# Kernel tuning notes

Hardware: AMD Instinct MI355X
Metric: run time of the kernel (lower is better)

## Reference

```python
import jax, jax.numpy as jnp
import numpy as np

NH = 8      # num_head
WIN = 7     # window
EPS = 1e-6


def _ln(x, w, b):
    m = x.mean(-1, keepdims=True)
    v = ((x - m) ** 2).mean(-1, keepdims=True)
    return (x - m) / jnp.sqrt(v + EPS) * w + b


def _dwconv(x, w, b):
    # x: [B,H,W,Cc], w: [7,7,1,Cc] (HWIO), depthwise (groups=Cc)
    y = jax.lax.conv_general_dilated(
        x, w, window_strides=(1, 1), padding='SAME',
        dimension_numbers=('NHWC', 'HWIO', 'NHWC'),
        feature_group_count=x.shape[-1])
    return y + b


def setup_inputs() -> dict:
    B, H, W, C = 16, 56, 56, 256
    RATIO = 8
    key = jax.random.key(0)
    ki = iter(jax.random.split(key, 48))
    def lin(i, o):
        return jax.random.normal(next(ki), (i, o), jnp.float32) * (1.0 / i) ** 0.5
    def bias(o):
        return jnp.zeros((o,), jnp.float32)
    def dw(c):
        return jax.random.normal(next(ki), (7, 7, 1, c), jnp.float32) * 0.05
    inp = {
        'x':   jax.random.normal(next(ki), (B, H, W, C), jnp.float32),
        'x_e': jax.random.normal(next(ki), (B, H, W, C // 2), jnp.float32),
        # LayerNorms
        'norm_w': jnp.ones((C,), jnp.float32),  'norm_b': bias(C),
        'norme_w': jnp.ones((C // 2,), jnp.float32), 'norme_b': bias(C // 2),
        # local_rr path
        'rr1_w': lin(C, C), 'rr1_b': bias(C),
        'rr2_w': lin(C, C), 'rr2_b': bias(C),
        'rr3_w': lin(C, C), 'rr3_b': bias(C),
        'conv_w': dw(C), 'conv_b': bias(C),
        # LocalAttentionRGBT
        'lx_l1_w': lin(C, C // 2), 'lx_l1_b': bias(C // 2),
        'lx_l2_w': lin(C // 2, C // 2), 'lx_l2_b': bias(C // 2),
        'lx_c1_w': dw(C // 2), 'lx_c1_b': bias(C // 2),
        'lx_c2_w': dw(C // 2), 'lx_c2_b': bias(C // 2),
        'lx_fc1_w': lin(C, C // RATIO),  # no bias
        'lx_fc2_w': lin(C // RATIO, C),  # no bias
        'lx_l3_w': lin(C, C // 2), 'lx_l3_b': bias(C // 2),
        # global pooled attention
        'kv_w': lin(C, C), 'kv_b': bias(C),
        'q_w': lin(C // 2 * 3, C // 2), 'q_b': bias(C // 2),
        # output projections (window != 0 => in = 2C)
        'proj_w': lin(2 * C, C), 'proj_b': bias(C),
        'proje_w': lin(2 * C, C // 2), 'proje_b': bias(C // 2),
    }
    return inp


def reference(x, x_e, norm_w, norm_b, norme_w, norme_b,
              rr1_w, rr1_b, rr2_w, rr2_b, rr3_w, rr3_b, conv_w, conv_b,
              lx_l1_w, lx_l1_b, lx_l2_w, lx_l2_b, lx_c1_w, lx_c1_b,
              lx_c2_w, lx_c2_b, lx_fc1_w, lx_fc2_w, lx_l3_w, lx_l3_b,
              kv_w, kv_b, q_w, q_b, proj_w, proj_b, proje_w, proje_b):
    B, H, W, C = x.shape
    hd = C // NH // 2  # head dim
    x = _ln(x, norm_w, norm_b)
    x_e = _ln(x_e, norme_w, norme_b)

    # --- local_rr: gated depthwise-conv branch ---
    rr1 = x @ rr1_w + rr1_b
    rr2 = _dwconv(x @ rr2_w + rr2_b, conv_w, conv_b)
    rr2 = rr2 @ rr3_w + rr3_b
    local_rr = rr1 * rr2  # [B,H,W,C]

    # --- LocalAttentionRGBT: cross-modal cosine-sim channel gate ---
    rgb = x @ lx_l1_w + lx_l1_b      # [B,H,W,C/2]
    t = x_e @ lx_l2_w + lx_l2_b      # [B,H,W,C/2]
    co = _dwconv(rgb * t, lx_c1_w, lx_c1_b)
    di = _dwconv(jnp.abs(rgb - t), lx_c2_w, lx_c2_b)
    co_di = jnp.concatenate([co, di], axis=-1)           # [B,H,W,C]
    amap = co_di.mean(-1, keepdims=True)                 # [B,H,W,1]
    dot = (amap * co_di).sum((1, 2), keepdims=True)      # [B,1,1,C]
    n1 = jnp.sqrt((amap ** 2).sum((1, 2), keepdims=True))
    n2 = jnp.sqrt((co_di ** 2).sum((1, 2), keepdims=True))
    cos_sim = dot / (n1 * n2 + 1e-6)                     # [B,1,1,C]
    attn_c = jax.nn.sigmoid(
        jax.nn.gelu(cos_sim @ lx_fc1_w, approximate=False) @ lx_fc2_w)
    local_rx = (co_di * attn_c) @ lx_l3_w + lx_l3_b      # [B,H,W,C/2]

    # --- global: pooled-q full-kv attention ---
    kv = (x @ kv_w + kv_b).reshape(B, H * W, 2, NH, hd).transpose(2, 0, 3, 1, 4)
    k, v = kv[0], kv[1]                                  # [B,NH,HW,hd]
    rx = jnp.concatenate([x, x_e], axis=-1)              # [B,H,W,3C/2]
    rx_pool = rx.reshape(B, WIN, H // WIN, WIN, W // WIN, -1).mean((2, 4))  # [B,7,7,3C/2]
    q = (rx_pool @ q_w + q_b).reshape(B, WIN * WIN, NH, hd).transpose(0, 2, 1, 3)
    scores = jnp.einsum('bnqd,bnkd->bnqk', q * hd ** -0.5, k)  # [B,NH,49,HW]
    attn = jax.nn.softmax(scores, axis=-1)
    g = jnp.einsum('bnqk,bnkd->bnqd', attn, v)           # [B,NH,49,hd]
    g = g.reshape(B, NH, WIN, WIN, hd).transpose(0, 1, 4, 2, 3).reshape(B, C // 2, WIN, WIN)
    g = jax.image.resize(g, (B, C // 2, H, W), method='bilinear')  # align_corners=False
    g = g.transpose(0, 2, 3, 1)                          # [B,H,W,C/2]

    cat = jnp.concatenate([local_rr, local_rx, g], axis=-1)  # [B,H,W,2C]
    x_e_out = cat @ proje_w + proje_b
    x_out = cat @ proj_w + proj_b
    return (x_out, x_e_out)
```

## Files before the change

### kernel.cpp

```cpp
#include <hip/hip_runtime.h>
#include <hip/hip_bf16.h>
#include <cstdint>
#include <cstddef>

#define N_TOK 50176
#define HWSZ  3136
#define BATCH 16

#define GF_MUL     1
#define GF_ASCALE  2
#define GF_KVSPLIT 4
#define GF_DUAL    8

typedef __hip_bfloat16 bf16;
typedef __attribute__((ext_vector_type(8))) short bf16x8;
typedef __attribute__((ext_vector_type(4))) float f32x4;
typedef __attribute__((ext_vector_type(4))) unsigned short u16x4;

__device__ __forceinline__ void  stf(float* p, size_t i, float v) { p[i] = v; }
__device__ __forceinline__ void  stf(bf16* p, size_t i, float v) { p[i] = __float2bfloat16(v); }
__device__ __forceinline__ float bu2f(unsigned short u) {
    unsigned int x = ((unsigned int)u) << 16; float f; __builtin_memcpy(&f, &x, 4); return f;
}
__device__ __forceinline__ unsigned short f2bu(float f) {
    bf16 t = __float2bfloat16(f); unsigned short u; __builtin_memcpy(&u, &t, 2); return u;
}

struct WtrDesc { const float* src; bf16* dst; int K; int N; int off; };
struct WtrPack { WtrDesc d[9]; int total; };
__global__ __launch_bounds__(256) void wtr_all(WtrPack p)
{
    int idx = blockIdx.x * 256 + threadIdx.x;
    if (idx >= p.total) return;
    #pragma unroll
    for (int s = 0; s < 9; s++) {
        int lo = p.d[s].off, hi = lo + p.d[s].K * p.d[s].N;
        if (idx >= lo && idx < hi) {
            int j = idx - lo;
            int k = j / p.d[s].N, n = j % p.d[s].N;
            p.d[s].dst[(size_t)n * p.d[s].K + k] = __float2bfloat16(p.d[s].src[j]);
        }
    }
}

__global__ __launch_bounds__(256) void ln_kernel(const float* __restrict__ in,
    const float* __restrict__ w, const float* __restrict__ b,
    bf16* __restrict__ out, int rows, int Cdim)
{
    int wave = threadIdx.x >> 6, lane = threadIdx.x & 63;
    int row = blockIdx.x * 4 + wave;
    if (row >= rows) return;
    const float* p = in + (size_t)row * Cdim;
    int nj = Cdim >> 6;
    float v[4];
    float s = 0.f;
    for (int j = 0; j < nj; j++) { v[j] = p[lane + 64 * j]; s += v[j]; }
    for (int off = 32; off; off >>= 1) s += __shfl_xor(s, off, 64);
    float mean = s / (float)Cdim;
    float vs = 0.f;
    for (int j = 0; j < nj; j++) { float d = v[j] - mean; vs += d * d; }
    for (int off = 32; off; off >>= 1) vs += __shfl_xor(vs, off, 64);
    float rstd = 1.f / sqrtf(vs / (float)Cdim + 1e-6f);
    bf16* q = out + (size_t)row * Cdim;
    for (int j = 0; j < nj; j++) {
        int c = lane + 64 * j;
        q[c] = __float2bfloat16((v[j] - mean) * rstd * w[c] + b[c]);
    }
}

#define LDT 56
template<int FLAGS, typename OT>
__global__ __launch_bounds__(256) void gemm_mfma(
    const bf16* __restrict__ A, int lda,
    const bf16* __restrict__ WT,
    const float* __restrict__ bias,
    OT* __restrict__ C, int ldc,
    int M, int K, int N,
    const bf16* __restrict__ mul, int mulld,
    const float* __restrict__ ascale,
    bf16* __restrict__ kout, bf16* __restrict__ vout,
    OT* __restrict__ C2, int ldc2, const float* __restrict__ bias2, int N1)
{
    __shared__ bf16 As[128][LDT];
    __shared__ bf16 Bs[128][LDT];
    int ntile = N >> 7;
    int m0 = (blockIdx.x / ntile) * 128;
    int n0 = (blockIdx.x % ntile) * 128;
    int tid = threadIdx.x;
    int lane = tid & 63, wid = tid >> 6;
    int wr = (wid >> 1) * 64, wc = (wid & 1) * 64;
    int lrow = lane & 15, lko = (lane >> 4) * 8;
    int sr = tid >> 2, sko = (tid & 3) * 8;

    f32x4 acc[4][4];
    #pragma unroll
    for (int i = 0; i < 4; i++)
        #pragma unroll
        for (int j = 0; j < 4; j++)
            acc[i][j] = (f32x4){0.f, 0.f, 0.f, 0.f};

    bf16x8 ra[2], rb[2];
    #pragma unroll
    for (int i = 0; i < 2; i++) {
        int r = sr + i * 64;
        bf16x8 v = *reinterpret_cast<const bf16x8*>(A + (size_t)(m0 + r) * lda + sko);
        if (FLAGS & GF_ASCALE) {
            int bidx = (m0 + r) / HWSZ;
            const float* as = ascale + (size_t)bidx * K + sko;
            #pragma unroll
            for (int e = 0; e < 8; e++)
                v[e] = (short)f2bu(bu2f((unsigned short)v[e]) * as[e]);
        }
        ra[i] = v;
        rb[i] = *reinterpret_cast<const bf16x8*>(WT + (size_t)(n0 + r) * K + sko);
    }

    for (int k0 = 0; k0 < K; k0 += 32) {
        #pragma unroll
        for (int i = 0; i < 2; i++) {
            *reinterpret_cast<bf16x8*>(&As[sr + i * 64][sko]) = ra[i];
            *reinterpret_cast<bf16x8*>(&Bs[sr + i * 64][sko]) = rb[i];
        }
        __syncthreads();
        int kn = k0 + 32;
        if (kn < K) {
            #pragma unroll
            for (int i = 0; i < 2; i++) {
                int r = sr + i * 64;
                bf16x8 v = *reinterpret_cast<const bf16x8*>(A + (size_t)(m0 + r) * lda + kn + sko);
                if (FLAGS & GF_ASCALE) {
                    int bidx = (m0 + r) / HWSZ;
                    const float* as = ascale + (size_t)bidx * K + kn + sko;
                    #pragma unroll
                    for (int e = 0; e < 8; e++)
                        v[e] = (short)f2bu(bu2f((unsigned short)v[e]) * as[e]);
                }
                ra[i] = v;
                rb[i] = *reinterpret_cast<const bf16x8*>(WT + (size_t)(n0 + r) * K + kn + sko);
            }
        }
        bf16x8 af[4], br[4];
        #pragma unroll
        for (int i = 0; i < 4; i++)
            af[i] = *reinterpret_cast<const bf16x8*>(&As[wr + i * 16 + lrow][lko]);
        #pragma unroll
        for (int j = 0; j < 4; j++)
            br[j] = *reinterpret_cast<const bf16x8*>(&Bs[wc + j * 16 + lrow][lko]);
        #pragma unroll
        for (int i = 0; i < 4; i++)
            #pragma unroll
            for (int j = 0; j < 4; j++)
                acc[i][j] = __builtin_amdgcn_mfma_f32_16x16x32_bf16(af[i], br[j], acc[i][j], 0, 0, 0);
        __syncthreads();
    }

    int orow = (lane >> 4) * 4;
    int ocol = lane & 15;
    #pragma unroll
    for (int i = 0; i < 4; i++) {
        #pragma unroll
        for (int j = 0; j < 4; j++) {
            #pragma unroll
            for (int p = 0; p < 4; p++) {
                int gm = m0 + wr + i * 16 + orow + p;
                int gn = n0 + wc + j * 16 + ocol;
                if (FLAGS & GF_KVSPLIT) {
                    float v = acc[i][j][p] + bias[gn];
                    int bb = gm / HWSZ, n = gm % HWSZ;
                    if (gn < 128)
                        kout[(((size_t)bb * 8 + (gn >> 4)) * HWSZ + n) * 16 + (gn & 15)] = __float2bfloat16(v);
                    else {
                        int hh = (gn - 128) >> 4, dd = (gn - 128) & 15;
                        vout[(((size_t)bb * 8 + hh) * 16 + dd) * HWSZ + n] = __float2bfloat16(v);
                    }
                } else if (FLAGS & GF_DUAL) {
                    if (gn < N1) {
                        float v = acc[i][j][p] + bias[gn];
                        stf(C, (size_t)gm * ldc + gn, v);
                    } else {
                        float v = acc[i][j][p] + bias2[gn - N1];
                        stf(C2, (size_t)gm * ldc2 + (gn - N1), v);
                    }
                } else {
                    float v = acc[i][j][p] + bias[gn];
                    if (FLAGS & GF_MUL) v *= __bfloat162float(mul[(size_t)gm * mulld + gn]);
                    stf(C, (size_t)gm * ldc + gn, v);
                }
            }
        }
    }
}

__global__ __launch_bounds__(256) void gemm_k(
    const float* __restrict__ A, int lda,
    const float* __restrict__ Wt, const float* __restrict__ bias,
    float* __restrict__ Cc, int ldc, int M, int K, int Nc)
{
    __shared__ float As[16][68];
    __shared__ float Ws[16][64];
    int ntile = Nc >> 6;
    int tile_n = blockIdx.x % ntile;
    int tile_m = blockIdx.x / ntile;
    int m0 = tile_m * 64, n0 = tile_n * 64;
    int tid = threadIdx.x;
    int tx = tid & 15, ty = tid >> 4;
    float acc[4][4] = {};
    for (int k0 = 0; k0 < K; k0 += 16) {
        int ks = tid & 15, ms = tid >> 4;
        #pragma unroll
        for (int i = 0; i < 4; i++) {
            int gm = m0 + ms + i * 16;
            As[ks][ms + i * 16] = (gm < M) ? A[(size_t)gm * lda + k0 + ks] : 0.f;
        }
        #pragma unroll
        for (int j = 0; j < 4; j++) {
            int k = (tid >> 6) * 4 + j;
            Ws[k][tid & 63] = Wt[(size_t)(k0 + k) * Nc + n0 + (tid & 63)];
        }
        __syncthreads();
        #pragma unroll
        for (int k = 0; k < 16; k++) {
            float a[4], w[4];
            #pragma unroll
            for (int i = 0; i < 4; i++) a[i] = As[k][ty * 4 + i];
            #pragma unroll
            for (int j = 0; j < 4; j++) w[j] = Ws[k][tx * 4 + j];
            #pragma unroll
            for (int i = 0; i < 4; i++)
                #pragma unroll
                for (int j = 0; j < 4; j++)
                    acc[i][j] += a[i] * w[j];
        }
        __syncthreads();
    }
    #pragma unroll
    for (int i = 0; i < 4; i++) {
        int gm = m0 + ty * 4 + i;
        if (gm >= M) continue;
        #pragma unroll
        for (int j = 0; j < 4; j++) {
            int gn = n0 + tx * 4 + j;
            Cc[(size_t)gm * ldc + gn] = acc[i][j] + bias[gn];
        }
    }
}

__global__ __launch_bounds__(256) void dwconv_reg(const bf16* __restrict__ in,
    bf16* __restrict__ out,
    const float* __restrict__ w0, const float* __restrict__ b0,
    const float* __restrict__ w1, const float* __restrict__ b1, int split)
{
    int tid = threadIdx.x;
    int chg = tid & 31;
    int bsw = (blockIdx.x & 7) * 196 + (blockIdx.x >> 3);
    int pg  = bsw * 8 + (tid >> 5);
    int xg = pg % 14;
    int y  = (pg / 14) % 56;
    int b  = pg / (14 * 56);
    int c0 = chg * 8;
    int x0 = xg * 4;

    const float* wp; const float* bp; int ws, cw;
    if (c0 < split) { wp = w0; bp = b0; ws = split;       cw = c0; }
    else            { wp = w1; bp = b1; ws = 256 - split; cw = c0 - split; }

    float acc[4][8];
    #pragma unroll
    for (int o = 0; o < 4; o++)
        #pragma unroll
        for (int e = 0; e < 8; e++) acc[o][e] = 0.f;

    const bf16* base = in + (size_t)b * HWSZ * 256 + c0;
    const float* wbase = wp + cw;
    #pragma unroll
    for (int ky = 0; ky < 7; ky++) {
        int gy = y + ky - 3;
        if (gy < 0 || gy >= 56) continue;
        const bf16* rowp = base + (size_t)gy * 56 * 256;
        float cf[10][8];
        #pragma unroll
        for (int j = 0; j < 10; j++) {
            int gx = x0 + j - 3;
            bf16x8 v = {0, 0, 0, 0, 0, 0, 0, 0};
            if ((unsigned)gx < 56u)
                v = *reinterpret_cast<const bf16x8*>(rowp + (size_t)gx * 256);
            #pragma unroll
            for (int e = 0; e < 8; e++) cf[j][e] = bu2f((unsigned short)v[e]);
        }
        const float* wrow = wbase + ky * 7 * ws;
        #pragma unroll
        for (int kx = 0; kx < 7; kx++) {
            float4 wa = *reinterpret_cast<const float4*>(wrow + kx * ws);
            float4 wb = *reinterpret_cast<const float4*>(wrow + kx * ws + 4);
            #pragma unroll
            for (int o = 0; o < 4; o++) {
                acc[o][0] += cf[o + kx][0] * wa.x;
                acc[o][1] += cf[o + kx][1] * wa.y;
                acc[o][2] += cf[o + kx][2] * wa.z;
                acc[o][3] += cf[o + kx][3] * wa.w;
                acc[o][4] += cf[o + kx][4] * wb.x;
                acc[o][5] += cf[o + kx][5] * wb.y;
                acc[o][6] += cf[o + kx][6] * wb.z;
                acc[o][7] += cf[o + kx][7] * wb.w;
            }
        }
    }

    float4 ba = *reinterpret_cast<const float4*>(bp + cw);
    float4 bb = *reinterpret_cast<const float4*>(bp + cw + 4);
    bf16* obase = out + (((size_t)b * HWSZ + (size_t)y * 56 + x0) * 256) + c0;
    #pragma unroll
    for (int o = 0; o < 4; o++) {
        bf16x8 ov;
        ov[0] = (short)f2bu(acc[o][0] + ba.x);
        ov[1] = (short)f2bu(acc[o][1] + ba.y);
        ov[2] = (short)f2bu(acc[o][2] + ba.z);
        ov[3] = (short)f2bu(acc[o][3] + ba.w);
        ov[4] = (short)f2bu(acc[o][4] + bb.x);
        ov[5] = (short)f2bu(acc[o][5] + bb.y);
        ov[6] = (short)f2bu(acc[o][6] + bb.z);
        ov[7] = (short)f2bu(acc[o][7] + bb.w);
        *reinterpret_cast<bf16x8*>(obase + (size_t)o * 256) = ov;
    }
}

__global__ void rgbt_k(const bf16* __restrict__ rgb, const bf16* __restrict__ t,
                       bf16* __restrict__ codin, int total )
{
    int i = blockIdx.x * blockDim.x + threadIdx.x;
    if (i >= total) return;
    int n = i >> 7, c = i & 127;
    float a = __bfloat162float(rgb[i]), bb = __bfloat162float(t[i]);
    codin[(size_t)n * 256 + c] = __float2bfloat16(a * bb);
    codin[(size_t)n * 256 + 128 + c] = __float2bfloat16(fabsf(a - bb));
}

__global__ __launch_bounds__(256) void cosred_k(const bf16* __restrict__ codi,
    float* __restrict__ part)
{
    int b = blockIdx.x >> 4;
    int bi = blockIdx.x & 15;
    int wave = threadIdx.x >> 6, lane = threadIdx.x & 63;
    int slot = bi * 4 + wave;
    float dloc[4] = {0,0,0,0}, n2loc[4] = {0,0,0,0};
    float n1loc = 0.f;
    for (int i = 0; i < 49; i++) {
        int p = slot * 49 + i;
        const bf16* row = codi + ((size_t)b * HWSZ + p) * 256;
        float v[4]; float sum = 0.f;
        #pragma unroll
        for (int j = 0; j < 4; j++) { v[j] = __bfloat162float(row[lane + 64 * j]); sum += v[j]; }
        for (int off = 32; off; off >>= 1) sum += __shfl_xor(sum, off, 64);
        float amap = sum * (1.f / 256.f);
        #pragma unroll
        for (int j = 0; j < 4; j++) { dloc[j] += amap * v[j]; n2loc[j] += v[j] * v[j]; }
        n1loc += amap * amap;
    }
    float* dst = part + ((size_t)b * 64 + slot) * 513;
    #pragma unroll
    for (int j = 0; j < 4; j++) {
        dst[lane + 64 * j] = dloc[j];
        dst[256 + lane + 64 * j] = n2loc[j];
    }
    if (lane == 0) dst[512] = n1loc;
}

__global__ __launch_bounds__(256) void mlp_kernel(const float* __restrict__ part,
    const float* __restrict__ fc1w, const float* __restrict__ fc2w,
    float* __restrict__ attnc)
{
    int b = blockIdx.x;
    int tid = threadIdx.x;
    __shared__ float cosb[256];
    __shared__ float hbuf[32];
    const float* pb = part + (size_t)b * 64 * 513;
    float dot = 0.f, n2 = 0.f, n1 = 0.f;
    for (int s = 0; s < 64; s++) {
        dot += pb[s * 513 + tid];
        n2  += pb[s * 513 + 256 + tid];
        n1  += pb[s * 513 + 512];
    }
    float cs = dot / (sqrtf(n1) * sqrtf(n2) + 1e-6f);
    cosb[tid] = cs;
    __syncthreads();
    if (tid < 32) {
        float h = 0.f;
        for (int c = 0; c < 256; c++) h += cosb[c] * fc1w[c * 32 + tid];
        h = 0.5f * h * (1.f + erff(h * 0.70710678f));
        hbuf[tid] = h;
    }
    __syncthreads();
    float o = 0.f;
    for (int j = 0; j < 32; j++) o += hbuf[j] * fc2w[j * 256 + tid];
    attnc[b * 256 + tid] = 1.f / (1.f + expf(-o));
}

__global__ __launch_bounds__(384) void pool_kernel(const bf16* __restrict__ xn,
    const bf16* __restrict__ xen, float* __restrict__ rxpool)
{
    int bij = blockIdx.x;
    int b = bij / 49; int ij = bij % 49; int i = ij / 7, j = ij % 7;
    int c = threadIdx.x;
    float s = 0.f;
    for (int dy = 0; dy < 8; dy++)
        for (int dx = 0; dx < 8; dx++) {
            size_t n = ((size_t)b * 56 + (i * 8 + dy)) * 56 + (j * 8 + dx);
            s += (c < 256) ? __bfloat162float(xn[n * 256 + c])
                           : __bfloat162float(xen[n * 128 + (c - 256)]);
        }
    rxpool[(size_t)bij * 384 + c] = s * (1.f / 64.f);
}

#define NSPLIT 14
#define POSB   224
__global__ __launch_bounds__(256) void attn_mfma(const float* __restrict__ qbuf,
    const bf16* __restrict__ kbuf, const bf16* __restrict__ vtbuf,
    float* __restrict__ osplit, float* __restrict__ mlbuf)
{
    int bh = blockIdx.x & 127;
    int split = blockIdx.x >> 7;
    int b = bh >> 3, h = bh & 7;
    int tid = threadIdx.x;
    int qt = tid >> 6;
    int lane = tid & 63;
    int lo = lane & 15, hi = lane >> 4;

    bf16x8 qf = {0, 0, 0, 0, 0, 0, 0, 0};
    int q = qt * 16 + lo;
    if (hi < 2 && q < 49) {
        const float* qp = qbuf + ((size_t)b * 49 + q) * 128 + h * 16 + hi * 8;
        #pragma unroll
        for (int j = 0; j < 8; j++) qf[j] = (short)f2bu(qp[j] * 0.25f);
    }
    const bf16* kbase = kbuf + (size_t)bh * HWSZ * 16;
    const bf16* vbase = vtbuf + ((size_t)bh * 16 + lo) * HWSZ;

    float m_run = -1e30f, l_run = 0.f;
    f32x4 oacc = {0.f, 0.f, 0.f, 0.f};
    int pos1 = 8 * (lo >> 2) + (lo & 3);
    const f32x4 zz = {0.f, 0.f, 0.f, 0.f};

    for (int t = 0; t < POSB / 32; t++) {
        int base = split * POSB + t * 32;
        bf16x8 kf1 = {0, 0, 0, 0, 0, 0, 0, 0}, kf2 = kf1;
        if (hi < 2) {
            kf1 = *reinterpret_cast<const bf16x8*>(kbase + (size_t)(base + pos1) * 16 + hi * 8);
            kf2 = *reinterpret_cast<const bf16x8*>(kbase + (size_t)(base + pos1 + 4) * 16 + hi * 8);
        }
        bf16x8 vf = *reinterpret_cast<const bf16x8*>(vbase + base + hi * 8);
        f32x4 s1 = __builtin_amdgcn_mfma_f32_16x16x32_bf16(kf1, qf, zz, 0, 0, 0);
        f32x4 s2 = __builtin_amdgcn_mfma_f32_16x16x32_bf16(kf2, qf, zz, 0, 0, 0);
        float pmax = fmaxf(fmaxf(fmaxf(s1[0], s1[1]), fmaxf(s1[2], s1[3])),
                           fmaxf(fmaxf(s2[0], s2[1]), fmaxf(s2[2], s2[3])));
        pmax = fmaxf(pmax, __shfl_xor(pmax, 16, 64));
        pmax = fmaxf(pmax, __shfl_xor(pmax, 32, 64));
        float mnew = fmaxf(m_run, pmax);
        float esc = __expf(m_run - mnew);
        l_run *= esc;
        float e0 = __shfl(esc, 4 * hi + 0, 64);
        float e1 = __shfl(esc, 4 * hi + 1, 64);
        float e2 = __shfl(esc, 4 * hi + 2, 64);
        float e3 = __shfl(esc, 4 * hi + 3, 64);
        oacc[0] *= e0; oacc[1] *= e1; oacc[2] *= e2; oacc[3] *= e3;
        float p0 = __expf(s1[0] - mnew), p1 = __expf(s1[1] - mnew);
        float p2 = __expf(s1[2] - mnew), p3 = __expf(s1[3] - mnew);
        float p4 = __expf(s2[0] - mnew), p5 = __expf(s2[1] - mnew);
        float p6 = __expf(s2[2] - mnew), p7 = __expf(s2[3] - mnew);
        float rs = ((p0 + p1) + (p2 + p3)) + ((p4 + p5) + (p6 + p7));
        rs += __shfl_xor(rs, 16, 64);
        rs += __shfl_xor(rs, 32, 64);
        l_run += rs;
        m_run = mnew;
        bf16x8 pf;
        pf[0] = (short)f2bu(p0); pf[1] = (short)f2bu(p1);
        pf[2] = (short)f2bu(p2); pf[3] = (short)f2bu(p3);
        pf[4] = (short)f2bu(p4); pf[5] = (short)f2bu(p5);
        pf[6] = (short)f2bu(p6); pf[7] = (short)f2bu(p7);
        oacc = __builtin_amdgcn_mfma_f32_16x16x32_bf16(pf, vf, oacc, 0, 0, 0);
    }

    float* ob = osplit + ((size_t)bh * NSPLIT + split) * 64 * 16;
    #pragma unroll
    for (int r = 0; r < 4; r++) {
        int qq = qt * 16 + 4 * hi + r;
        ob[(size_t)qq * 16 + lo] = oacc[r];
    }
    if (hi == 0) {
        float* mlb = mlbuf + (((size_t)bh * NSPLIT + split) * 64 + qt * 16 + lo) * 2;
        mlb[0] = m_run; mlb[1] = l_run;
    }
}

__global__ __launch_bounds__(256) void attn_combine(const float* __restrict__ osplit,
    const float* __restrict__ mlbuf, float* __restrict__ gs)
{
    int idx = blockIdx.x * 256 + threadIdx.x;
    if (idx >= 128 * 49 * 16) return;
    int d = idx & 15;
    int pq = idx >> 4;
    int bh = pq / 49, q = pq % 49;
    float m[NSPLIT], l[NSPLIT];
    float M = -1e30f;
    #pragma unroll
    for (int s = 0; s < NSPLIT; s++) {
        const float* mlb = mlbuf + (((size_t)bh * NSPLIT + s) * 64 + q) * 2;
        m[s] = mlb[0]; l[s] = mlb[1];
        M = fmaxf(M, m[s]);
    }
    float L = 0.f, O = 0.f;
    #pragma unroll
    for (int s = 0; s < NSPLIT; s++) {
        float e = __expf(m[s] - M);
        L += l[s] * e;
        O += osplit[(((size_t)bh * NSPLIT + s) * 64 + q) * 16 + d] * e;
    }
    gs[(size_t)pq * 16 + d] = O / L;
}

__global__ void upsample_kernel(const float* __restrict__ gs, bf16* __restrict__ cat)
{
    int idx = blockIdx.x * blockDim.x + threadIdx.x;
    if (idx >= N_TOK * 128) return;
    int c = idx & 127;
    int pos = idx >> 7;
    int h = c >> 4, d = c & 15;
    int x = pos % 56;
    int y = (pos / 56) % 56;
    int b = pos / HWSZ;
    float sy = (y + 0.5f) * 0.125f - 0.5f;
    float sx = (x + 0.5f) * 0.125f - 0.5f;
    int y0f = (int)floorf(sy); float wy = sy - (float)y0f;
    int x0f = (int)floorf(sx); float wx = sx - (float)x0f;
    int y0 = max(0, min(6, y0f)), y1 = max(0, min(6, y0f + 1));
    int x0 = max(0, min(6, x0f)), x1 = max(0, min(6, x0f + 1));
    const float* g0 = gs + ((size_t)(b * 8 + h) * 49) * 16 + d;
    float v00 = g0[(y0 * 7 + x0) * 16], v01 = g0[(y0 * 7 + x1) * 16];
    float v10 = g0[(y1 * 7 + x0) * 16], v11 = g0[(y1 * 7 + x1) * 16];
    float v0 = v00 + (v01 - v00) * wx;
    float v1 = v10 + (v11 - v10) * wx;
    float v = v0 + (v1 - v0) * wy;
    cat[(size_t)pos * 512 + 384 + c] = __float2bfloat16(v);
}

extern "C" void kernel_launch(void* const* d_in, const int* in_sizes, int n_in,
                              void* d_out, int out_size, void* d_ws, size_t ws_size,
                              hipStream_t stream)
{
    const float* x      = (const float*)d_in[0];
    const float* x_e    = (const float*)d_in[1];
    const float* norm_w = (const float*)d_in[2];
    const float* norm_b = (const float*)d_in[3];
    const float* norme_w= (const float*)d_in[4];
    const float* norme_b= (const float*)d_in[5];
    const float* rr1_w  = (const float*)d_in[6];
    const float* rr1_b  = (const float*)d_in[7];
    const float* rr2_w  = (const float*)d_in[8];
    const float* rr2_b  = (const float*)d_in[9];
    const float* rr3_w  = (const float*)d_in[10];
    const float* rr3_b  = (const float*)d_in[11];
    const float* conv_w = (const float*)d_in[12];
    const float* conv_b = (const float*)d_in[13];
    const float* l1_w   = (const float*)d_in[14];
    const float* l1_b   = (const float*)d_in[15];
    const float* l2_w   = (const float*)d_in[16];
    const float* l2_b   = (const float*)d_in[17];
    const float* c1_w   = (const float*)d_in[18];
    const float* c1_b   = (const float*)d_in[19];
    const float* c2_w   = (const float*)d_in[20];
    const float* c2_b   = (const float*)d_in[21];
    const float* fc1_w  = (const float*)d_in[22];
    const float* fc2_w  = (const float*)d_in[23];
    const float* l3_w   = (const float*)d_in[24];
    const float* l3_b   = (const float*)d_in[25];
    const float* kv_w   = (const float*)d_in[26];
    const float* kv_b   = (const float*)d_in[27];
    const float* q_w    = (const float*)d_in[28];
    const float* q_b    = (const float*)d_in[29];
    const float* proj_w = (const float*)d_in[30];
    const float* proj_b = (const float*)d_in[31];
    const float* proje_w= (const float*)d_in[32];
    const float* proje_b= (const float*)d_in[33];

    float* part   = (float*)d_ws;
    float* attnc  = part   + (size_t)525312;
    float* gs     = attnc  + 4096;
    float* rxpool = gs     + 100352;
    float* qbuf   = rxpool + 301056;
    bf16* wt      = (bf16*)(qbuf + 100352);
    bf16* rr1_t  = wt;
    bf16* rr2_t  = rr1_t + 65536;
    bf16* rr3_t  = rr2_t + 65536;
    bf16* kv_t   = rr3_t + 65536;
    bf16* l1_t   = kv_t  + 65536;
    bf16* l2_t   = l1_t  + 32768;
    bf16* l3_t   = l2_t  + 16384;
    bf16* proj_t = l3_t  + 32768;
    bf16* proje_t= proj_t + 131072;
    bf16* xn     = proje_t + 65536;
    bf16* xen    = xn   + (size_t)N_TOK * 256;
    bf16* bufC   = xen  + (size_t)N_TOK * 128;
    bf16* bufD   = bufC + (size_t)N_TOK * 256;
    bf16* bufE   = bufD + (size_t)N_TOK * 256;
    bf16* cat    = bufE + (size_t)N_TOK * 256;
    size_t need = (size_t)((char*)(cat + (size_t)N_TOK * 512) - (char*)d_ws);
    if (ws_size < need) return;

    bf16* kbuf = bufC;
    bf16* vbuf = bufC + (size_t)N_TOK * 128;

    float* osplit = (float*)bufD;
    float* mlbuf  = osplit + (size_t)128 * NSPLIT * 64 * 16;

    float* xout  = (float*)d_out;
    float* xeout = xout + (size_t)N_TOK * 256;

    const int nthr = 256;
    auto mgrid = [](int M, int N) { return dim3((M / 128) * (N / 128)); };

    {
        WtrPack p;
        const float* srcs[9] = {rr1_w, rr2_w, rr3_w, kv_w, l1_w, l2_w, l3_w, proj_w, proje_w};
        bf16* dsts[9] = {rr1_t, rr2_t, rr3_t, kv_t, l1_t, l2_t, l3_t, proj_t, proje_t};
        int Ks[9] = {256, 256, 256, 256, 256, 128, 256, 512, 512};
        int Ns[9] = {256, 256, 256, 256, 128, 128, 128, 256, 128};
        int off = 0;
        for (int s = 0; s < 9; s++) {
            p.d[s] = {srcs[s], dsts[s], Ks[s], Ns[s], off};
            off += Ks[s] * Ns[s];
        }
        p.total = off;
        wtr_all<<<dim3((off + 255) / 256), dim3(256), 0, stream>>>(p);
    }

    ln_kernel<<<dim3(N_TOK / 4), dim3(nthr), 0, stream>>>(x, norm_w, norm_b, xn, N_TOK, 256);
    ln_kernel<<<dim3(N_TOK / 4), dim3(nthr), 0, stream>>>(x_e, norme_w, norme_b, xen, N_TOK, 128);

    gemm_mfma<GF_DUAL, bf16><<<mgrid(N_TOK, 512), dim3(nthr), 0, stream>>>(
        xn, 256, rr1_t, rr1_b, bufC, 256, N_TOK, 256, 512, nullptr, 0, nullptr, nullptr, nullptr,
        bufD, 256, rr2_b, 256);
    dwconv_reg<<<dim3(N_TOK / 32), dim3(nthr), 0, stream>>>(
        bufD, bufE, conv_w, conv_b, conv_w, conv_b, 256);
    gemm_mfma<GF_MUL, bf16><<<mgrid(N_TOK, 256), dim3(nthr), 0, stream>>>(
        bufE, 256, rr3_t, rr3_b, cat, 512, N_TOK, 256, 256, bufC, 256, nullptr, nullptr, nullptr,
        nullptr, 0, nullptr, 0);

    gemm_mfma<0, bf16><<<mgrid(N_TOK, 128), dim3(nthr), 0, stream>>>(
        xn, 256, l1_t, l1_b, bufD, 128, N_TOK, 256, 128, nullptr, 0, nullptr, nullptr, nullptr,
        nullptr, 0, nullptr, 0);
    gemm_mfma<0, bf16><<<mgrid(N_TOK, 128), dim3(nthr), 0, stream>>>(
        xen, 128, l2_t, l2_b, bufD + (size_t)N_TOK * 128, 128, N_TOK, 128, 128, nullptr, 0, nullptr, nullptr, nullptr,
        nullptr, 0, nullptr, 0);
    rgbt_k<<<dim3((N_TOK * 128) / nthr), dim3(nthr), 0, stream>>>(
        bufD, bufD + (size_t)N_TOK * 128, bufC, N_TOK * 128);
    dwconv_reg<<<dim3(N_TOK / 32), dim3(nthr), 0, stream>>>(
        bufC, bufE, c1_w, c1_b, c2_w, c2_b, 128);
    cosred_k<<<dim3(BATCH * 16), dim3(nthr), 0, stream>>>(bufE, part);
    mlp_kernel<<<dim3(BATCH), dim3(nthr), 0, stream>>>(part, fc1_w, fc2_w, attnc);
    gemm_mfma<GF_ASCALE, bf16><<<mgrid(N_TOK, 128), dim3(nthr), 0, stream>>>(
        bufE, 256, l3_t, l3_b, cat + 256, 512, N_TOK, 256, 128, nullptr, 0, attnc, nullptr, nullptr,
        nullptr, 0, nullptr, 0);

    gemm_mfma<GF_KVSPLIT, bf16><<<mgrid(N_TOK, 256), dim3(nthr), 0, stream>>>(
        xn, 256, kv_t, kv_b, (bf16*)nullptr, 0, N_TOK, 256, 256, nullptr, 0, nullptr, kbuf, vbuf,
        nullptr, 0, nullptr, 0);
    pool_kernel<<<dim3(BATCH * 49), dim3(384), 0, stream>>>(xn, xen, rxpool);
    gemm_k<<<dim3(((784 + 63) / 64) * 2), dim3(nthr), 0, stream>>>(
        rxpool, 384, q_w, q_b, qbuf, 128, 784, 384, 128);
    attn_mfma<<<dim3(128 * NSPLIT), dim3(nthr), 0, stream>>>(qbuf, kbuf, vbuf, osplit, mlbuf);
    attn_combine<<<dim3(392), dim3(nthr), 0, stream>>>(osplit, mlbuf, gs);
    upsample_kernel<<<dim3((N_TOK * 128) / nthr), dim3(nthr), 0, stream>>>(gs, cat);

    gemm_mfma<GF_DUAL, float><<<mgrid(N_TOK, 384), dim3(nthr), 0, stream>>>(
        cat, 512, proj_t, proj_b, xout, 256, N_TOK, 512, 384, nullptr, 0, nullptr, nullptr, nullptr,
        xeout, 128, proje_b, 256);
}
```

Before: 451.2 us.

## Shrink GEMM tile to 64x128 and swizzle block order across XCDs

Halves the M-dimension of the MFMA GEMM tile from 128 to 64. Each wave now owns a 64x32 output slice instead of 64x64, and the grid is doubled accordingly. It also remaps block IDs so consecutive blocks are distributed in groups of 8, presumably to spread work across the chip's XCDs or improve cache locality. The smaller tile raises occupancy and block count but lowers per-block data reuse, and the swizzle assumes the grid is divisible by 8.

```diff
diff --git a/kernel.cpp b/kernel.cpp
--- a/kernel.cpp
+++ b/kernel.cpp
@@ -81,75 +81,71 @@
     bf16* __restrict__ kout, bf16* __restrict__ vout,
     OT* __restrict__ C2, int ldc2, const float* __restrict__ bias2, int N1)
 {
-    __shared__ bf16 As[128][LDT];
+    __shared__ bf16 As[64][LDT];
     __shared__ bf16 Bs[128][LDT];
     int ntile = N >> 7;
-    int m0 = (blockIdx.x / ntile) * 128;
-    int n0 = (blockIdx.x % ntile) * 128;
+    int bid = blockIdx.x;
+    bid = (bid & 7) * (gridDim.x >> 3) + (bid >> 3);
+    int m0 = (bid / ntile) * 64;
+    int n0 = (bid % ntile) * 128;
     int tid = threadIdx.x;
     int lane = tid & 63, wid = tid >> 6;
-    int wr = (wid >> 1) * 64, wc = (wid & 1) * 64;
+    int wc = wid * 32;
     int lrow = lane & 15, lko = (lane >> 4) * 8;
     int sr = tid >> 2, sko = (tid & 3) * 8;
 
-    f32x4 acc[4][4];
+    f32x4 acc[4][2];
     #pragma unroll
     for (int i = 0; i < 4; i++)
         #pragma unroll
-        for (int j = 0; j < 4; j++)
+        for (int j = 0; j < 2; j++)
             acc[i][j] = (f32x4){0.f, 0.f, 0.f, 0.f};
 
-    bf16x8 ra[2], rb[2];
-    #pragma unroll
-    for (int i = 0; i < 2; i++) {
-        int r = sr + i * 64;
-        bf16x8 v = *reinterpret_cast<const bf16x8*>(A + (size_t)(m0 + r) * lda + sko);
+    bf16x8 ra, rb[2];
+    {
+        bf16x8 v = *reinterpret_cast<const bf16x8*>(A + (size_t)(m0 + sr) * lda + sko);
         if (FLAGS & GF_ASCALE) {
-            int bidx = (m0 + r) / HWSZ;
+            int bidx = (m0 + sr) / HWSZ;
             const float* as = ascale + (size_t)bidx * K + sko;
             #pragma unroll
             for (int e = 0; e < 8; e++)
                 v[e] = (short)f2bu(bu2f((unsigned short)v[e]) * as[e]);
         }
-        ra[i] = v;
-        rb[i] = *reinterpret_cast<const bf16x8*>(WT + (size_t)(n0 + r) * K + sko);
+        ra = v;
+        rb[0] = *reinterpret_cast<const bf16x8*>(WT + (size_t)(n0 + sr) * K + sko);
+        rb[1] = *reinterpret_cast<const bf16x8*>(WT + (size_t)(n0 + sr + 64) * K + sko);
     }
 
     for (int k0 = 0; k0 < K; k0 += 32) {
-        #pragma unroll
-        for (int i = 0; i < 2; i++) {
-            *reinterpret_cast<bf16x8*>(&As[sr + i * 64][sko]) = ra[i];
-            *reinterpret_cast<bf16x8*>(&Bs[sr + i * 64][sko]) = rb[i];
-        }
+        *reinterpret_cast<bf16x8*>(&As[sr][sko]) = ra;
+        *reinterpret_cast<bf16x8*>(&Bs[sr][sko]) = rb[0];
+        *reinterpret_cast<bf16x8*>(&Bs[sr + 64][sko]) = rb[1];
         __syncthreads();
         int kn = k0 + 32;
         if (kn < K) {
-            #pragma unroll
-            for (int i = 0; i < 2; i++) {
-                int r = sr + i * 64;
-                bf16x8 v = *reinterpret_cast<const bf16x8*>(A + (size_t)(m0 + r) * lda + kn + sko);
-                if (FLAGS & GF_ASCALE) {
-                    int bidx = (m0 + r) / HWSZ;
-                    const float* as = ascale + (size_t)bidx * K + kn + sko;
-                    #pragma unroll
-                    for (int e = 0; e < 8; e++)
-                        v[e] = (short)f2bu(bu2f((unsigned short)v[e]) * as[e]);
-                }
-                ra[i] = v;
-                rb[i] = *reinterpret_cast<const bf16x8*>(WT + (size_t)(n0 + r) * K + kn + sko);
+            bf16x8 v = *reinterpret_cast<const bf16x8*>(A + (size_t)(m0 + sr) * lda + kn + sko);
+            if (FLAGS & GF_ASCALE) {
+                int bidx = (m0 + sr) / HWSZ;
+                const float* as = ascale + (size_t)bidx * K + kn + sko;
+                #pragma unroll
+                for (int e = 0; e < 8; e++)
+                    v[e] = (short)f2bu(bu2f((unsigned short)v[e]) * as[e]);
             }
-        }
-        bf16x8 af[4], br[4];
+            ra = v;
+            rb[0] = *reinterpret_cast<const bf16x8*>(WT + (size_t)(n0 + sr) * K + kn + sko);
+            rb[1] = *reinterpret_cast<const bf16x8*>(WT + (size_t)(n0 + sr + 64) * K + kn + sko);
+        }
+        bf16x8 af[4], br[2];
         #pragma unroll
         for (int i = 0; i < 4; i++)
-            af[i] = *reinterpret_cast<const bf16x8*>(&As[wr + i * 16 + lrow][lko]);
-        #pragma unroll
-        for (int j = 0; j < 4; j++)
+            af[i] = *reinterpret_cast<const bf16x8*>(&As[i * 16 + lrow][lko]);
+        #pragma unroll
+        for (int j = 0; j < 2; j++)
             br[j] = *reinterpret_cast<const bf16x8*>(&Bs[wc + j * 16 + lrow][lko]);
         #pragma unroll
         for (int i = 0; i < 4; i++)
             #pragma unroll
-            for (int j = 0; j < 4; j++)
+            for (int j = 0; j < 2; j++)
                 acc[i][j] = __builtin_amdgcn_mfma_f32_16x16x32_bf16(af[i], br[j], acc[i][j], 0, 0, 0);
         __syncthreads();
     }
@@ -159,10 +155,10 @@
     #pragma unroll
     for (int i = 0; i < 4; i++) {
         #pragma unroll
-        for (int j = 0; j < 4; j++) {
+        for (int j = 0; j < 2; j++) {
             #pragma unroll
             for (int p = 0; p < 4; p++) {
-                int gm = m0 + wr + i * 16 + orow + p;
+                int gm = m0 + i * 16 + orow + p;
                 int gn = n0 + wc + j * 16 + ocol;
                 if (FLAGS & GF_KVSPLIT) {
                     float v = acc[i][j][p] + bias[gn];
@@ -615,7 +611,7 @@
     float* xeout = xout + (size_t)N_TOK * 256;
 
     const int nthr = 256;
-    auto mgrid = [](int M, int N) { return dim3((M / 128) * (N / 128)); };
+    auto mgrid = [](int M, int N) { return dim3((M / 64) * (N / 128)); };
 
     {
         WtrPack p;
```

Result: faster. 433.9 us (-3.8%).
